# Kernel tuning notes

Hardware: AMD Instinct MI355X
Metric: run time of the kernel (lower is better)

The kernel has to match this reference:

```python
import jax, jax.numpy as jnp
import numpy as np

B, N, D, NS, ITERS = 64, 4096, 256, 8, 3
EPS_ATTN = 1e-5   # module eps (added to attn)
EPS_LN = 1e-5     # torch LayerNorm default eps


def layer_norm(x, g, b):
    m = jnp.mean(x, axis=-1, keepdims=True)
    v = jnp.mean((x - m) ** 2, axis=-1, keepdims=True)
    return (x - m) / jnp.sqrt(v + EPS_LN) * g + b


def setup_inputs() -> dict:
    key = jax.random.key(0)
    ks = jax.random.split(key, 16)
    s = 0.02
    return {
        "inputs": jax.random.normal(ks[0], (B, N, D), jnp.float32),
        "slots_init": jax.random.normal(ks[1], (1, NS, D), jnp.float32),
        "Wq": jax.random.normal(ks[2], (D, D), jnp.float32) * s,
        "Wk": jax.random.normal(ks[3], (D, D), jnp.float32) * s,
        "Wv": jax.random.normal(ks[4], (D, D), jnp.float32) * s,
        "W_ih": jax.random.normal(ks[5], (3 * D, D), jnp.float32) * s,
        "W_hh": jax.random.normal(ks[6], (3 * D, D), jnp.float32) * s,
        "b_ih": jnp.zeros((3 * D,), jnp.float32),
        "b_hh": jnp.zeros((3 * D,), jnp.float32),
        "ln_in_g": jnp.ones((D,), jnp.float32),
        "ln_in_b": jnp.zeros((D,), jnp.float32),
        "ln_s_g": jnp.ones((D,), jnp.float32),
        "ln_s_b": jnp.zeros((D,), jnp.float32),
        "ln_m_g": jnp.ones((D,), jnp.float32),
        "ln_m_b": jnp.zeros((D,), jnp.float32),
        "W1": jax.random.normal(ks[7], (4 * D, D), jnp.float32) * s,
        "b1": jnp.zeros((4 * D,), jnp.float32),
        "W2": jax.random.normal(ks[8], (D, 4 * D), jnp.float32) * s,
        "b2": jnp.zeros((D,), jnp.float32),
    }


def gru_cell(x, h, W_ih, W_hh, b_ih, b_hh):
    # x, h: [M, D]; PyTorch GRU cell equations (gate order r, z, n)
    gi = x @ W_ih.T + b_ih
    gh = h @ W_hh.T + b_hh
    gi_r, gi_z, gi_n = jnp.split(gi, 3, axis=-1)
    gh_r, gh_z, gh_n = jnp.split(gh, 3, axis=-1)
    r = jax.nn.sigmoid(gi_r + gh_r)
    z = jax.nn.sigmoid(gi_z + gh_z)
    n = jnp.tanh(gi_n + r * gh_n)
    return (1.0 - z) * n + z * h


def reference(inputs, slots_init, Wq, Wk, Wv, W_ih, W_hh, b_ih, b_hh,
              ln_in_g, ln_in_b, ln_s_g, ln_s_b, ln_m_g, ln_m_b,
              W1, b1, W2, b2):
    b, n, d = inputs.shape
    scale = d ** -0.5
    slots = jnp.broadcast_to(slots_init, (b, NS, d))

    x = layer_norm(inputs, ln_in_g, ln_in_b)
    k = x @ Wk.T  # [b, n, d]
    v = x @ Wv.T  # [b, n, d]

    for _ in range(ITERS):
        slots_prev = slots
        s_n = layer_norm(slots, ln_s_g, ln_s_b)
        q = s_n @ Wq.T  # [b, ns, d]
        dots = jnp.einsum('bid,bjd->bij', q, k) * scale  # [b, ns, n]
        attn = jax.nn.softmax(dots, axis=1) + EPS_ATTN   # softmax over slots
        attn = attn / jnp.mean(attn, axis=-1, keepdims=True)
        updates = jnp.einsum('bjd,bij->bid', v, attn)     # [b, ns, d]
        h = gru_cell(updates.reshape(-1, d), slots_prev.reshape(-1, d),
                     W_ih, W_hh, b_ih, b_hh)
        slots = h.reshape(b, NS, d)
        # residual MLP with pre-norm
        y = layer_norm(slots, ln_m_g, ln_m_b)
        y = jax.nn.leaky_relu(y @ W1.T + b1, negative_slope=0.01)
        slots = slots + (y @ W2.T + b2)
    return slots
```

## Files before the change

### kernel.cpp

```cpp
#include <hip/hip_runtime.h>
#include <hip/hip_fp16.h>
#include <hip/hip_bf16.h>


#define BB 64
#define NN 4096
#define DD 256
#define NSL 8
#define NITER 3

__device__ __forceinline__ float wredsum(float v){
#pragma unroll
  for(int m=32;m;m>>=1) v += __shfl_xor(v, m, 64);
  return v;
}
__device__ __forceinline__ float2 u2f2(unsigned u){ __half2 h; __builtin_memcpy(&h,&u,4); return __half22float2(h); }
__device__ __forceinline__ float sigm(float v){ return 1.0f/(1.0f+__expf(-v)); }

union U4 { uint4 u; __half2 h[4]; };

__global__ __launch_bounds__(256) void k_prep(
    const float* __restrict__ Whh, const float* __restrict__ W1,
    const float* __restrict__ W2,  const float* __restrict__ sinit,
    __half* __restrict__ Wg, __half* __restrict__ W1t, __half* __restrict__ W2t,
    float* __restrict__ slots){
  for(int idx=blockIdx.x*256+threadIdx.x; idx<851968; idx+=gridDim.x*256){
    if(idx<196608){ int col=idx>>8, c=idx&255; Wg[(size_t)c*1536+768+col]=__float2half(Whh[idx]); }
    else if(idx<458752){ int k=idx-196608; int col=k>>8, c=k&255; W1t[(size_t)c*1024+col]=__float2half(W1[k]); }
    else if(idx<720896){ int k=idx-458752; int col=k>>10, c=k&1023; W2t[(size_t)c*256+col]=__float2half(W2[k]); }
    else { int k=idx-720896; slots[k]=sinit[k&2047]; }
  }
}

__global__ __launch_bounds__(256) void k_WC(const float* __restrict__ Wih, const float* __restrict__ Wv,
                                            __half* __restrict__ Wg){
  int col=blockIdx.x;
  int t=threadIdx.x;
  __shared__ float wr[256];
  wr[t]=Wih[col*256+t];
  __syncthreads();
  float acc=0.f;
#pragma unroll 8
  for(int d=0;d<256;d++) acc += wr[d]*Wv[d*256+t];
  Wg[(size_t)t*1536+col]=__float2half(acc);
}

__global__ __launch_bounds__(256) void k_M(const float* __restrict__ Wq, const float* __restrict__ Wk,
                                           __half* __restrict__ M2h){
  int c = blockIdx.x, e = threadIdx.x;
  float acc = 0.f;
#pragma unroll 8
  for(int d=0; d<256; d++) acc += Wq[d*256+e]*Wk[d*256+c];
  M2h[c*256+e] = __float2half(acc * 0.0625f);
}

__global__ __launch_bounds__(256) void k_ln_x(const float* __restrict__ in, const float* __restrict__ g,
                                              const float* __restrict__ bbv, __half* __restrict__ x){
  int row  = blockIdx.x*4 + (threadIdx.x>>6);
  int lane = threadIdx.x&63;
  const float4 v = ((const float4*)(in + (size_t)row*DD))[lane];
  float s  = v.x+v.y+v.z+v.w;
  float ss = v.x*v.x+v.y*v.y+v.z*v.z+v.w*v.w;
  s = wredsum(s); ss = wredsum(ss);
  float m = s*(1.0f/256.0f);
  float r = rsqrtf(ss*(1.0f/256.0f) - m*m + 1e-5f);
  float4 gv = ((const float4*)g)[lane];
  float4 bv = ((const float4*)bbv)[lane];
  float y0=(v.x-m)*r*gv.x+bv.x, y1=(v.y-m)*r*gv.y+bv.y;
  float y2=(v.z-m)*r*gv.z+bv.z, y3=(v.w-m)*r*gv.w+bv.w;
  __half2 h0=__floats2half2_rn(y0,y1), h1=__floats2half2_rn(y2,y3);
  uint2 u; __builtin_memcpy(&u.x,&h0,4); __builtin_memcpy(&u.y,&h1,4);
  ((uint2*)(x + (size_t)row*DD))[lane] = u;
}

__global__ __launch_bounds__(256) void k_pre(const float* __restrict__ slots, const float* __restrict__ g,
                                             const float* __restrict__ bbv, const __half* __restrict__ M2h,
                                             float* __restrict__ qs){
  int row = blockIdx.x;
  int t = threadIdx.x;
  __shared__ __align__(16) float sn[256];
  __shared__ float red[8];
  float v = slots[row*256 + t];
  float s = wredsum(v), ss = wredsum(v*v);
  int wid=t>>6, lane=t&63;
  if(lane==0){ red[wid]=s; red[4+wid]=ss; }
  __syncthreads();
  float S  = red[0]+red[1]+red[2]+red[3];
  float SS = red[4]+red[5]+red[6]+red[7];
  float m = S*(1.0f/256.0f);
  float r = rsqrtf(SS*(1.0f/256.0f) - m*m + 1e-5f);
  sn[t] = (v-m)*r*g[t]+bbv[t];
  __syncthreads();
  const uint4* w4 = (const uint4*)(M2h + (size_t)t*256);
  float acc=0.f;
#pragma unroll 4
  for(int kk=0;kk<32;kk++){
    U4 w; w.u=w4[kk];
#pragma unroll
    for(int q=0;q<4;q++){
      float2 f=__half22float2(w.h[q]);
      acc += sn[kk*8+2*q]*f.x + sn[kk*8+2*q+1]*f.y;
    }
  }
  qs[row*256+t]=acc;
}

__global__ __launch_bounds__(256) void k_att(const __half* __restrict__ x, const float* __restrict__ qs,
                                             float* __restrict__ pagg){
  int b = blockIdx.x>>4;
  int t = threadIdx.x;
  size_t j = (size_t)blockIdx.x*256 + t;
  __shared__ __align__(16) float qt[256][8];
  __shared__ __align__(16) float wl[256][8];
  __shared__ __align__(16) float aggl[4][2048];
  __shared__ float wsl[4][8];
  const float* qb = qs + b*2048;
  for(int e=t;e<2048;e+=256) qt[e&255][e>>8]=qb[e];
  __syncthreads();
  const uint4* xr = (const uint4*)(x + j*DD);
  float pd[8]={0,0,0,0,0,0,0,0};
#pragma unroll 2
  for(int ch=0; ch<32; ch++){
    uint4 u = xr[ch];
    float2 f0=u2f2(u.x), f1=u2f2(u.y), f2=u2f2(u.z), f3=u2f2(u.w);
    float xv[8]={f0.x,f0.y,f1.x,f1.y,f2.x,f2.y,f3.x,f3.y};
    int c0=ch*8;
#pragma unroll
    for(int cc=0;cc<8;cc++){
      const float4* qp=(const float4*)&qt[c0+cc][0];
      float4 qa=qp[0], qc=qp[1];
      float xvv=xv[cc];
      pd[0]+=qa.x*xvv; pd[1]+=qa.y*xvv; pd[2]+=qa.z*xvv; pd[3]+=qa.w*xvv;
      pd[4]+=qc.x*xvv; pd[5]+=qc.y*xvv; pd[6]+=qc.z*xvv; pd[7]+=qc.w*xvv;
    }
  }
  float mx=pd[0];
#pragma unroll
  for(int i=1;i<8;i++) mx=fmaxf(mx,pd[i]);
  float ev[8]; float ssum=0.f;
#pragma unroll
  for(int i=0;i<8;i++){ ev[i]=__expf(pd[i]-mx); ssum+=ev[i]; }
  float inv=1.0f/ssum;
#pragma unroll
  for(int i=0;i<8;i++) wl[t][i]=ev[i]*inv+1e-5f;
  __syncthreads();
  int wid=t>>6, lane=t&63;
  float acc[8][4];
#pragma unroll
  for(int i=0;i<8;i++){ acc[i][0]=0;acc[i][1]=0;acc[i][2]=0;acc[i][3]=0; }
  float ws[8]={0,0,0,0,0,0,0,0};
  for(int r=0;r<64;r++){
    int jl = wid*64 + r;
    uint2 u = ((const uint2*)(x + ((size_t)blockIdx.x*256 + jl)*DD))[lane];
    float2 f01=u2f2(u.x), f23=u2f2(u.y);
    const float4* wp=(const float4*)&wl[jl][0];
    float4 wa=wp[0], wb_=wp[1];
    float wv[8]={wa.x,wa.y,wa.z,wa.w,wb_.x,wb_.y,wb_.z,wb_.w};
    float xv[4]={f01.x,f01.y,f23.x,f23.y};
#pragma unroll
    for(int i=0;i<8;i++){
      acc[i][0]+=wv[i]*xv[0]; acc[i][1]+=wv[i]*xv[1];
      acc[i][2]+=wv[i]*xv[2]; acc[i][3]+=wv[i]*xv[3];
      ws[i]+=wv[i];
    }
  }
#pragma unroll
  for(int i=0;i<8;i++){
    float4 st={acc[i][0],acc[i][1],acc[i][2],acc[i][3]};
    *((float4*)&aggl[wid][i*256 + lane*4])=st;
  }
  if(lane==0){
#pragma unroll
    for(int i=0;i<8;i++) wsl[wid][i]=ws[i];
  }
  __syncthreads();
  float* pb = pagg + (size_t)blockIdx.x*2064;
  for(int e=t;e<2048;e+=256) pb[e]=aggl[0][e]+aggl[1][e]+aggl[2][e]+aggl[3][e];
  if(t<8) pb[2048+t]=wsl[0][t]+wsl[1][t]+wsl[2][t]+wsl[3][t];
}

__global__ __launch_bounds__(512) void t_gates2(
    const float* __restrict__ pagg, const float* __restrict__ slots_in,
    const __half* __restrict__ Wg, const float* __restrict__ bih, const float* __restrict__ bhh,
    const float* __restrict__ lm_g, const float* __restrict__ lm_b,
    float* __restrict__ hb, __half* __restrict__ ysh){
  int row0=blockIdx.x*2;
  int b=row0>>3, i0=row0&7;
  int t=threadIdx.x;
  int r=t>>8, c=t&255;
  __shared__ float AS[4][256];
  __shared__ __align__(16) float gl[2][1536];
  __shared__ float fac[2];
  __shared__ float redS[2][4], redQ[2][4];
  const float* pb = pagg + (size_t)b*16*2064;
  {
    float s=0.f;
#pragma unroll
    for(int ch=0;ch<16;ch++) s += pb[ch*2064 + (i0+r)*256 + c];
    AS[r][c]=s;
    AS[2+r][c]=slots_in[(size_t)(row0+r)*256+c];
  }
  if(t<2){
    float s=0.f;
#pragma unroll
    for(int ch=0;ch<16;ch++) s += pb[ch*2064 + 2048 + i0 + t];
    fac[t]=4096.0f/s;
  }
  __syncthreads();
  AS[r][c] *= fac[r];
  __syncthreads();
  if(t<384){
    int c0=t*4;
    bool ih = c0<768;
    const float* X0 = ih? AS[0] : AS[2];
    const float* X1 = ih? AS[1] : AS[3];
    const __half* wb = Wg + c0;
    float a00=0,a01=0,a02=0,a03=0, a10=0,a11=0,a12=0,a13=0;
#pragma unroll 8
    for(int k=0;k<256;k++){
      uint2 u = *(const uint2*)(wb + (size_t)k*1536);
      float2 f0=u2f2(u.x), f1=u2f2(u.y);
      float x0=X0[k], x1=X1[k];
      a00+=x0*f0.x; a01+=x0*f0.y; a02+=x0*f1.x; a03+=x0*f1.y;
      a10+=x1*f0.x; a11+=x1*f0.y; a12+=x1*f1.x; a13+=x1*f1.y;
    }
    const float* bb = ih? bih : bhh;
    int bc = ih? c0 : c0-768;
    float4 bv=*(const float4*)&bb[bc];
    gl[0][c0]=a00+bv.x; gl[0][c0+1]=a01+bv.y; gl[0][c0+2]=a02+bv.z; gl[0][c0+3]=a03+bv.w;
    gl[1][c0]=a10+bv.x; gl[1][c0+1]=a11+bv.y; gl[1][c0+2]=a12+bv.z; gl[1][c0+3]=a13+bv.w;
  }
  __syncthreads();
  {
    float gir=gl[r][c], giz=gl[r][256+c], gin=gl[r][512+c];
    float ghr=gl[r][768+c], ghz=gl[r][1024+c], ghn=gl[r][1280+c];
    float hp=AS[2+r][c];
    float rr=sigm(gir+ghr), z=sigm(giz+ghz);
    float n=tanhf(gin+rr*ghn);
    float hv=(1.0f-z)*n+z*hp;
    hb[(size_t)(row0+r)*256+c]=hv;
    float s=wredsum(hv), ss=wredsum(hv*hv);
    if((t&63)==0){ redS[r][(t>>6)&3]=s; redQ[r][(t>>6)&3]=ss; }
    __syncthreads();
    float S_=redS[r][0]+redS[r][1]+redS[r][2]+redS[r][3];
    float SS=redQ[r][0]+redQ[r][1]+redQ[r][2]+redQ[r][3];
    float m=S_*(1.0f/256.0f);
    float rs=rsqrtf(SS*(1.0f/256.0f)-m*m+1e-5f);
    ysh[(size_t)(row0+r)*256+c]=__float2half((hv-m)*rs*lm_g[c]+lm_b[c]);
  }
}

__global__ __launch_bounds__(512) void t_mlp(
    const float* __restrict__ hb, const __half* __restrict__ ysg,
    const __half* __restrict__ W1t, const float* __restrict__ b1,
    const __half* __restrict__ W2t, const float* __restrict__ b2,
    const float* __restrict__ ls_g, const float* __restrict__ ls_b,
    const __half* __restrict__ M2h,
    float* __restrict__ dst, float* __restrict__ qs, int last){
  int row0=blockIdx.x*2;
  int t=threadIdx.x;
  int r=t>>8, c=t&255;
  __shared__ float ys[2][256];
  __shared__ __align__(16) float pz[2][2][1024];
  __shared__ __align__(16) float z1[2][1024];
  __shared__ float pm[2][4][256];
  __shared__ float redS[2][4], redQ[2][4];
  ys[r][c]=__half2float(ysg[(size_t)(row0+r)*256+c]);
  __syncthreads();
  {
    int c0=c*4;
    const __half* wb = W1t + (size_t)r*128*1024 + c0;
    float a00=0,a01=0,a02=0,a03=0, a10=0,a11=0,a12=0,a13=0;
#pragma unroll 8
    for(int k=0;k<128;k++){
      uint2 u=*(const uint2*)(wb + (size_t)k*1024);
      float2 f0=u2f2(u.x), f1=u2f2(u.y);
      float x0=ys[0][r*128+k], x1=ys[1][r*128+k];
      a00+=x0*f0.x; a01+=x0*f0.y; a02+=x0*f1.x; a03+=x0*f1.y;
      a10+=x1*f0.x; a11+=x1*f0.y; a12+=x1*f1.x; a13+=x1*f1.y;
    }
    pz[r][0][c0]=a00; pz[r][0][c0+1]=a01; pz[r][0][c0+2]=a02; pz[r][0][c0+3]=a03;
    pz[r][1][c0]=a10; pz[r][1][c0+1]=a11; pz[r][1][c0+2]=a12; pz[r][1][c0+3]=a13;
  }
  __syncthreads();
  for(int idx=t; idx<2048; idx+=512){
    int rr2=idx>>10, cc=idx&1023;
    float v=pz[0][rr2][cc]+pz[1][rr2][cc]+b1[cc];
    z1[rr2][cc]= v>0.f? v : 0.01f*v;
  }
  __syncthreads();
  if(t<256){
    int ks4=t>>6, cg=t&63;
    int c0=cg*4;
    const __half* wb = W2t + (size_t)ks4*256*256 + c0;
    float a00=0,a01=0,a02=0,a03=0, a10=0,a11=0,a12=0,a13=0;
#pragma unroll 8
    for(int k=0;k<256;k++){
      uint2 u=*(const uint2*)(wb + (size_t)k*256);
      float2 f0=u2f2(u.x), f1=u2f2(u.y);
      float x0=z1[0][ks4*256+k], x1=z1[1][ks4*256+k];
      a00+=x0*f0.x; a01+=x0*f0.y; a02+=x0*f1.x; a03+=x0*f1.y;
      a10+=x1*f0.x; a11+=x1*f0.y; a12+=x1*f1.x; a13+=x1*f1.y;
    }
    pm[0][ks4][c0]=a00; pm[0][ks4][c0+1]=a01; pm[0][ks4][c0+2]=a02; pm[0][ks4][c0+3]=a03;
    pm[1][ks4][c0]=a10; pm[1][ks4][c0+1]=a11; pm[1][ks4][c0+2]=a12; pm[1][ks4][c0+3]=a13;
  }
  __syncthreads();
  float s = hb[(size_t)(row0+r)*256+c] + pm[r][0][c]+pm[r][1][c]+pm[r][2][c]+pm[r][3][c] + b2[c];
  dst[(size_t)(row0+r)*256+c]=s;
  if(last) return;
  float su=wredsum(s), sq=wredsum(s*s);
  if((t&63)==0){ redS[r][(t>>6)&3]=su; redQ[r][(t>>6)&3]=sq; }
  __syncthreads();
  float S_=redS[r][0]+redS[r][1]+redS[r][2]+redS[r][3];
  float SS=redQ[r][0]+redQ[r][1]+redQ[r][2]+redQ[r][3];
  float m=S_*(1.0f/256.0f);
  float rs=rsqrtf(SS*(1.0f/256.0f)-m*m+1e-5f);
  ys[r][c]=(s-m)*rs*ls_g[c]+ls_b[c];
  __syncthreads();
  {
    const uint4* m4=(const uint4*)(M2h+(size_t)c*256);
    float acc=0.f;
#pragma unroll 4
    for(int kk=0;kk<32;kk++){
      U4 w; w.u=m4[kk];
#pragma unroll
      for(int q=0;q<4;q++){
        float2 f=__half22float2(w.h[q]);
        acc += ys[r][kk*8+2*q]*f.x + ys[r][kk*8+2*q+1]*f.y;
      }
    }
    qs[(size_t)(row0+r)*256+c]=acc;
  }
}

extern "C" void kernel_launch(void* const* d_in, const int* in_sizes, int n_in,
                              void* d_out, int out_size, void* d_ws, size_t ws_size,
                              hipStream_t stream){
  const float* inputs=(const float*)d_in[0];
  const float* sinit =(const float*)d_in[1];
  const float* Wq =(const float*)d_in[2];
  const float* Wk =(const float*)d_in[3];
  const float* Wv =(const float*)d_in[4];
  const float* Wih=(const float*)d_in[5];
  const float* Whh=(const float*)d_in[6];
  const float* bih=(const float*)d_in[7];
  const float* bhh=(const float*)d_in[8];
  const float* lin_g=(const float*)d_in[9];
  const float* lin_b=(const float*)d_in[10];
  const float* ls_g=(const float*)d_in[11];
  const float* ls_b=(const float*)d_in[12];
  const float* lm_g=(const float*)d_in[13];
  const float* lm_b=(const float*)d_in[14];
  const float* W1=(const float*)d_in[15];
  const float* b1=(const float*)d_in[16];
  const float* W2=(const float*)d_in[17];
  const float* b2=(const float*)d_in[18];

  char* w=(char*)d_ws;
  __half* x    =(__half*)w; w += (size_t)BB*NN*DD*2;
  float* qs    =(float*)w;  w += 512*256*4;
  float* slots =(float*)w;  w += 512*256*4;
  float* pagg  =(float*)w;  w += (size_t)1024*2064*4;
  __half* M2h  =(__half*)w; w += 256*256*2;
  __half* Wg   =(__half*)w; w += 256*1536*2;
  __half* W1t  =(__half*)w; w += 256*1024*2;
  __half* W2t  =(__half*)w; w += 1024*256*2;
  float* hb    =(float*)w;  w += 512*256*4;
  __half* ysh  =(__half*)w; w += 512*256*2;

  hipLaunchKernelGGL(k_prep, dim3(1664), dim3(256), 0, stream,
                     Whh, W1, W2, sinit, Wg, W1t, W2t, slots);
  hipLaunchKernelGGL(k_WC,   dim3(768),  dim3(256), 0, stream, Wih, Wv, Wg);
  hipLaunchKernelGGL(k_M,    dim3(256),  dim3(256), 0, stream, Wq, Wk, M2h);
  hipLaunchKernelGGL(k_ln_x, dim3(65536),dim3(256), 0, stream, inputs, lin_g, lin_b, x);
  hipLaunchKernelGGL(k_pre,  dim3(512),  dim3(256), 0, stream, slots, ls_g, ls_b, M2h, qs);
  for(int it=0; it<NITER; ++it){
    int last = (it==NITER-1);
    float* dst = last ? (float*)d_out : slots;
    hipLaunchKernelGGL(k_att,    dim3(1024), dim3(256), 0, stream, x, qs, pagg);
    hipLaunchKernelGGL(t_gates2, dim3(256),  dim3(512), 0, stream, pagg, slots, Wg, bih, bhh,
                       lm_g, lm_b, hb, ysh);
    hipLaunchKernelGGL(t_mlp,    dim3(256),  dim3(512), 0, stream, hb, ysh, W1t, b1, W2t, b2,
                       ls_g, ls_b, M2h, dst, qs, last);
  }
}
```

Baseline: 462.2 us.

## Fuse slot-attention iterations into one cooperative persistent kernel with grid syncs

Replaces the per-iteration k_att, t_gates2 and t_mlp launches plus k_pre with a single cooperative kernel. It uses grid.sync between the attention phase and the per-row GRU/MLP phase, and interleaves the weights into k-pair-major half2 layouts for coalesced per-thread column loads. The attention aggregation now loops over rows with a strided x column access per thread, and each block processes one slot row instead of two. This removes launch gaps and intermediate buffers, but grid syncs and fewer rows per block lower reuse of the weight loads.

```diff
diff --git a/kernel.cpp b/kernel.cpp
--- a/kernel.cpp
+++ b/kernel.cpp
@@ -1,6 +1,9 @@
 #include <hip/hip_runtime.h>
 #include <hip/hip_fp16.h>
 #include <hip/hip_bf16.h>
+#include <hip/hip_cooperative_groups.h>
+
+namespace cg = cooperative_groups;
 
 
 #define BB 64
@@ -17,23 +20,29 @@
 __device__ __forceinline__ float2 u2f2(unsigned u){ __half2 h; __builtin_memcpy(&h,&u,4); return __half22float2(h); }
 __device__ __forceinline__ float sigm(float v){ return 1.0f/(1.0f+__expf(-v)); }
 
-union U4 { uint4 u; __half2 h[4]; };
-
 __global__ __launch_bounds__(256) void k_prep(
     const float* __restrict__ Whh, const float* __restrict__ W1,
     const float* __restrict__ W2,  const float* __restrict__ sinit,
-    __half* __restrict__ Wg, __half* __restrict__ W1t, __half* __restrict__ W2t,
+    __half* __restrict__ Wgp, __half* __restrict__ W1p, __half* __restrict__ W2p,
     float* __restrict__ slots){
   for(int idx=blockIdx.x*256+threadIdx.x; idx<851968; idx+=gridDim.x*256){
-    if(idx<196608){ int col=idx>>8, c=idx&255; Wg[(size_t)c*1536+768+col]=__float2half(Whh[idx]); }
-    else if(idx<458752){ int k=idx-196608; int col=k>>8, c=k&255; W1t[(size_t)c*1024+col]=__float2half(W1[k]); }
-    else if(idx<720896){ int k=idx-458752; int col=k>>10, c=k&1023; W2t[(size_t)c*256+col]=__float2half(W2[k]); }
-    else { int k=idx-720896; slots[k]=sinit[k&2047]; }
+    if(idx<196608){
+      int col=idx>>8, k=idx&255; int g=3+(col>>8), c=col&255;
+      Wgp[(((size_t)g*128+(k>>1))*256+c)*2+(k&1)] = __float2half(Whh[idx]);
+    } else if(idx<458752){
+      int k2=idx-196608; int col=k2>>8, k=k2&255; int g=col>>8, c=col&255;
+      W1p[(((size_t)g*128+(k>>1))*256+c)*2+(k&1)] = __float2half(W1[k2]);
+    } else if(idx<720896){
+      int k3=idx-458752; int col=k3>>10, k=k3&1023;
+      W2p[(((size_t)(k>>1))*256+col)*2+(k&1)] = __float2half(W2[k3]);
+    } else {
+      int k4=idx-720896; slots[k4]=sinit[k4&2047];
+    }
   }
 }
 
 __global__ __launch_bounds__(256) void k_WC(const float* __restrict__ Wih, const float* __restrict__ Wv,
-                                            __half* __restrict__ Wg){
+                                            __half* __restrict__ Wgp){
   int col=blockIdx.x;
   int t=threadIdx.x;
   __shared__ float wr[256];
@@ -42,16 +51,17 @@
   float acc=0.f;
 #pragma unroll 8
   for(int d=0;d<256;d++) acc += wr[d]*Wv[d*256+t];
-  Wg[(size_t)t*1536+col]=__float2half(acc);
+  int g=col>>8, c=col&255;
+  Wgp[(((size_t)g*128+(t>>1))*256+c)*2+(t&1)] = __float2half(acc);
 }
 
 __global__ __launch_bounds__(256) void k_M(const float* __restrict__ Wq, const float* __restrict__ Wk,
-                                           __half* __restrict__ M2h){
+                                           __half* __restrict__ Mp){
   int c = blockIdx.x, e = threadIdx.x;
   float acc = 0.f;
 #pragma unroll 8
   for(int d=0; d<256; d++) acc += Wq[d*256+e]*Wk[d*256+c];
-  M2h[c*256+e] = __float2half(acc * 0.0625f);
+  Mp[(((size_t)(e>>1))*256+c)*2+(e&1)] = __float2half(acc * 0.0625f);
 }
 
 __global__ __launch_bounds__(256) void k_ln_x(const float* __restrict__ in, const float* __restrict__ g,
@@ -73,264 +83,201 @@
   ((uint2*)(x + (size_t)row*DD))[lane] = u;
 }
 
-__global__ __launch_bounds__(256) void k_pre(const float* __restrict__ slots, const float* __restrict__ g,
-                                             const float* __restrict__ bbv, const __half* __restrict__ M2h,
-                                             float* __restrict__ qs){
-  int row = blockIdx.x;
-  int t = threadIdx.x;
-  __shared__ __align__(16) float sn[256];
-  __shared__ float red[8];
-  float v = slots[row*256 + t];
-  float s = wredsum(v), ss = wredsum(v*v);
-  int wid=t>>6, lane=t&63;
-  if(lane==0){ red[wid]=s; red[4+wid]=ss; }
-  __syncthreads();
-  float S  = red[0]+red[1]+red[2]+red[3];
-  float SS = red[4]+red[5]+red[6]+red[7];
-  float m = S*(1.0f/256.0f);
-  float r = rsqrtf(SS*(1.0f/256.0f) - m*m + 1e-5f);
-  sn[t] = (v-m)*r*g[t]+bbv[t];
-  __syncthreads();
-  const uint4* w4 = (const uint4*)(M2h + (size_t)t*256);
-  float acc=0.f;
-#pragma unroll 4
-  for(int kk=0;kk<32;kk++){
-    U4 w; w.u=w4[kk];
-#pragma unroll
-    for(int q=0;q<4;q++){
-      float2 f=__half22float2(w.h[q]);
-      acc += sn[kk*8+2*q]*f.x + sn[kk*8+2*q+1]*f.y;
-    }
-  }
-  qs[row*256+t]=acc;
-}
-
-__global__ __launch_bounds__(256) void k_att(const __half* __restrict__ x, const float* __restrict__ qs,
-                                             float* __restrict__ pagg){
-  int b = blockIdx.x>>4;
-  int t = threadIdx.x;
-  size_t j = (size_t)blockIdx.x*256 + t;
+__global__ __launch_bounds__(256, 4) void k_main(
+    const __half* __restrict__ x, float* __restrict__ qs, float* __restrict__ slots,
+    float* __restrict__ pagg,
+    const __half* __restrict__ Wgp, const __half* __restrict__ W1p,
+    const __half* __restrict__ W2p, const __half* __restrict__ Mp,
+    const float* __restrict__ bih, const float* __restrict__ bhh,
+    const float* __restrict__ lm_g, const float* __restrict__ lm_b,
+    const float* __restrict__ b1, const float* __restrict__ b2,
+    const float* __restrict__ ls_g, const float* __restrict__ ls_b,
+    float* __restrict__ out){
+  cg::grid_group grid = cg::this_grid();
+  const int blk=blockIdx.x, t=threadIdx.x, G=gridDim.x;
+  const int wid=t>>6, lane=t&63;
   __shared__ __align__(16) float qt[256][8];
   __shared__ __align__(16) float wl[256][8];
-  __shared__ __align__(16) float aggl[4][2048];
   __shared__ float wsl[4][8];
-  const float* qb = qs + b*2048;
-  for(int e=t;e<2048;e+=256) qt[e&255][e>>8]=qb[e];
-  __syncthreads();
-  const uint4* xr = (const uint4*)(x + j*DD);
-  float pd[8]={0,0,0,0,0,0,0,0};
+  __shared__ float aggS[256], slS[256], ysl[256];
+  __shared__ __align__(16) float z1l[1024];
+  __shared__ float redS[4], redQ[4], facS, f16S[16];
+  const __half2* Wg2=(const __half2*)Wgp;
+  const __half2* W12=(const __half2*)W1p;
+  const __half2* W22=(const __half2*)W2p;
+  const __half2* Mp2=(const __half2*)Mp;
+
+  for(int row=blk; row<512; row+=G){
+    __syncthreads();
+    float v = slots[(size_t)row*256+t];
+    float s=wredsum(v), ss=wredsum(v*v);
+    if(lane==0){ redS[wid]=s; redQ[wid]=ss; }
+    __syncthreads();
+    float S=redS[0]+redS[1]+redS[2]+redS[3];
+    float SS=redQ[0]+redQ[1]+redQ[2]+redQ[3];
+    float m=S*(1.0f/256.0f);
+    float rs=rsqrtf(SS*(1.0f/256.0f)-m*m+1e-5f);
+    ysl[t]=(v-m)*rs*ls_g[t]+ls_b[t];
+    __syncthreads();
+    float acc=0.f;
+#pragma unroll 8
+    for(int k2=0;k2<128;k2++){
+      float2 f=__half22float2(Mp2[(size_t)k2*256+t]);
+      acc += f.x*ysl[2*k2] + f.y*ysl[2*k2+1];
+    }
+    qs[(size_t)row*256+t]=acc;
+  }
+  grid.sync();
+
+  for(int it=0; it<NITER; ++it){
+    const int last = (it==NITER-1);
+    for(int ab=blk; ab<1024; ab+=G){
+      __syncthreads();
+      int b = ab>>4;
+      const float* qb = qs + (size_t)b*2048;
+      for(int e=t;e<2048;e+=256) qt[e&255][e>>8]=qb[e];
+      __syncthreads();
+      size_t j = (size_t)ab*256 + t;
+      const uint4* xr = (const uint4*)(x + j*DD);
+      float pd[8]={0,0,0,0,0,0,0,0};
 #pragma unroll 2
-  for(int ch=0; ch<32; ch++){
-    uint4 u = xr[ch];
-    float2 f0=u2f2(u.x), f1=u2f2(u.y), f2=u2f2(u.z), f3=u2f2(u.w);
-    float xv[8]={f0.x,f0.y,f1.x,f1.y,f2.x,f2.y,f3.x,f3.y};
-    int c0=ch*8;
-#pragma unroll
-    for(int cc=0;cc<8;cc++){
-      const float4* qp=(const float4*)&qt[c0+cc][0];
-      float4 qa=qp[0], qc=qp[1];
-      float xvv=xv[cc];
-      pd[0]+=qa.x*xvv; pd[1]+=qa.y*xvv; pd[2]+=qa.z*xvv; pd[3]+=qa.w*xvv;
-      pd[4]+=qc.x*xvv; pd[5]+=qc.y*xvv; pd[6]+=qc.z*xvv; pd[7]+=qc.w*xvv;
+      for(int ch=0; ch<32; ch++){
+        uint4 u = xr[ch];
+        float2 f0=u2f2(u.x), f1=u2f2(u.y), f2=u2f2(u.z), f3=u2f2(u.w);
+        float xv[8]={f0.x,f0.y,f1.x,f1.y,f2.x,f2.y,f3.x,f3.y};
+        int c0=ch*8;
+#pragma unroll
+        for(int cc=0;cc<8;cc++){
+          const float4* qp=(const float4*)&qt[c0+cc][0];
+          float4 qa=qp[0], qc=qp[1];
+          float xvv=xv[cc];
+          pd[0]+=qa.x*xvv; pd[1]+=qa.y*xvv; pd[2]+=qa.z*xvv; pd[3]+=qa.w*xvv;
+          pd[4]+=qc.x*xvv; pd[5]+=qc.y*xvv; pd[6]+=qc.z*xvv; pd[7]+=qc.w*xvv;
+        }
+      }
+      float mx=pd[0];
+#pragma unroll
+      for(int i=1;i<8;i++) mx=fmaxf(mx,pd[i]);
+      float w[8]; float ssum=0.f;
+#pragma unroll
+      for(int i=0;i<8;i++){ w[i]=__expf(pd[i]-mx); ssum+=w[i]; }
+      float inv=1.0f/ssum;
+#pragma unroll
+      for(int i=0;i<8;i++){ w[i]=w[i]*inv+1e-5f; wl[t][i]=w[i]; }
+#pragma unroll
+      for(int i=0;i<8;i++){
+        float s=wredsum(w[i]);
+        if(lane==0) wsl[wid][i]=s;
+      }
+      __syncthreads();
+      if(t<8) pagg[(size_t)ab*2064 + 2048 + t] = wsl[0][t]+wsl[1][t]+wsl[2][t]+wsl[3][t];
+      int c = wid*64 + lane;
+      float acc[8]={0,0,0,0,0,0,0,0};
+      const __half* xb = x + (size_t)ab*256*DD + c;
+#pragma unroll 4
+      for(int j2=0;j2<256;j2++){
+        float xv = __half2float(xb[(size_t)j2*DD]);
+        const float4* wp=(const float4*)&wl[j2][0];
+        float4 w0=wp[0], w1=wp[1];
+        acc[0]+=w0.x*xv; acc[1]+=w0.y*xv; acc[2]+=w0.z*xv; acc[3]+=w0.w*xv;
+        acc[4]+=w1.x*xv; acc[5]+=w1.y*xv; acc[6]+=w1.z*xv; acc[7]+=w1.w*xv;
+      }
+#pragma unroll
+      for(int i=0;i<8;i++) pagg[(size_t)ab*2064 + i*256 + c] = acc[i];
     }
-  }
-  float mx=pd[0];
-#pragma unroll
-  for(int i=1;i<8;i++) mx=fmaxf(mx,pd[i]);
-  float ev[8]; float ssum=0.f;
-#pragma unroll
-  for(int i=0;i<8;i++){ ev[i]=__expf(pd[i]-mx); ssum+=ev[i]; }
-  float inv=1.0f/ssum;
-#pragma unroll
-  for(int i=0;i<8;i++) wl[t][i]=ev[i]*inv+1e-5f;
-  __syncthreads();
-  int wid=t>>6, lane=t&63;
-  float acc[8][4];
-#pragma unroll
-  for(int i=0;i<8;i++){ acc[i][0]=0;acc[i][1]=0;acc[i][2]=0;acc[i][3]=0; }
-  float ws[8]={0,0,0,0,0,0,0,0};
-  for(int r=0;r<64;r++){
-    int jl = wid*64 + r;
-    uint2 u = ((const uint2*)(x + ((size_t)blockIdx.x*256 + jl)*DD))[lane];
-    float2 f01=u2f2(u.x), f23=u2f2(u.y);
-    const float4* wp=(const float4*)&wl[jl][0];
-    float4 wa=wp[0], wb_=wp[1];
-    float wv[8]={wa.x,wa.y,wa.z,wa.w,wb_.x,wb_.y,wb_.z,wb_.w};
-    float xv[4]={f01.x,f01.y,f23.x,f23.y};
-#pragma unroll
-    for(int i=0;i<8;i++){
-      acc[i][0]+=wv[i]*xv[0]; acc[i][1]+=wv[i]*xv[1];
-      acc[i][2]+=wv[i]*xv[2]; acc[i][3]+=wv[i]*xv[3];
-      ws[i]+=wv[i];
+    grid.sync();
+    float* dst = last ? out : slots;
+    for(int row=blk; row<512; row+=G){
+      __syncthreads();
+      int b=row>>3, i0=row&7;
+      const float* pb = pagg + (size_t)b*16*2064;
+      float s=0.f;
+#pragma unroll
+      for(int ch=0;ch<16;ch++) s += pb[ch*2064 + i0*256 + t];
+      if(t<16) f16S[t]=pb[t*2064 + 2048 + i0];
+      float hp = slots[(size_t)row*256+t];
+      slS[t]=hp;
+      __syncthreads();
+      float wsum=0.f;
+#pragma unroll
+      for(int k2=0;k2<16;k2++) wsum+=f16S[k2];
+      aggS[t]=s*(4096.0f/wsum);
+      __syncthreads();
+      float a0=0,a1=0,a2=0,a3=0,a4=0,a5=0;
+#pragma unroll 8
+      for(int k2=0;k2<128;k2++){
+        float xa0=aggS[2*k2], xa1=aggS[2*k2+1];
+        float xs0=slS[2*k2],  xs1=slS[2*k2+1];
+        float2 f0=__half22float2(Wg2[(size_t)(0*128+k2)*256+t]);
+        float2 f1=__half22float2(Wg2[(size_t)(1*128+k2)*256+t]);
+        float2 f2=__half22float2(Wg2[(size_t)(2*128+k2)*256+t]);
+        float2 f3=__half22float2(Wg2[(size_t)(3*128+k2)*256+t]);
+        float2 f4=__half22float2(Wg2[(size_t)(4*128+k2)*256+t]);
+        float2 f5=__half22float2(Wg2[(size_t)(5*128+k2)*256+t]);
+        a0+=f0.x*xa0+f0.y*xa1; a1+=f1.x*xa0+f1.y*xa1; a2+=f2.x*xa0+f2.y*xa1;
+        a3+=f3.x*xs0+f3.y*xs1; a4+=f4.x*xs0+f4.y*xs1; a5+=f5.x*xs0+f5.y*xs1;
+      }
+      float gir=a0+bih[t], giz=a1+bih[256+t], gin=a2+bih[512+t];
+      float ghr=a3+bhh[t], ghz=a4+bhh[256+t], ghn=a5+bhh[512+t];
+      float rr=sigm(gir+ghr), z=sigm(giz+ghz);
+      float n=tanhf(gin+rr*ghn);
+      float hv=(1.0f-z)*n + z*hp;
+      float s1=wredsum(hv), q1=wredsum(hv*hv);
+      if(lane==0){ redS[wid]=s1; redQ[wid]=q1; }
+      __syncthreads();
+      float S=redS[0]+redS[1]+redS[2]+redS[3];
+      float SS=redQ[0]+redQ[1]+redQ[2]+redQ[3];
+      float m=S*(1.0f/256.0f);
+      float rs=rsqrtf(SS*(1.0f/256.0f)-m*m+1e-5f);
+      ysl[t]=(hv-m)*rs*lm_g[t]+lm_b[t];
+      __syncthreads();
+      float m0=0,m1=0,m2=0,m3=0;
+#pragma unroll 8
+      for(int k2=0;k2<128;k2++){
+        float y0=ysl[2*k2], y1=ysl[2*k2+1];
+        float2 f0=__half22float2(W12[(size_t)(0*128+k2)*256+t]);
+        float2 f1=__half22float2(W12[(size_t)(1*128+k2)*256+t]);
+        float2 f2=__half22float2(W12[(size_t)(2*128+k2)*256+t]);
+        float2 f3=__half22float2(W12[(size_t)(3*128+k2)*256+t]);
+        m0+=f0.x*y0+f0.y*y1; m1+=f1.x*y0+f1.y*y1;
+        m2+=f2.x*y0+f2.y*y1; m3+=f3.x*y0+f3.y*y1;
+      }
+      {
+        float v0=m0+b1[t];      z1l[t]      = v0>0.f?v0:0.01f*v0;
+        float v1=m1+b1[256+t];  z1l[256+t]  = v1>0.f?v1:0.01f*v1;
+        float v2=m2+b1[512+t];  z1l[512+t]  = v2>0.f?v2:0.01f*v2;
+        float v3=m3+b1[768+t];  z1l[768+t]  = v3>0.f?v3:0.01f*v3;
+      }
+      __syncthreads();
+      float o=0.f;
+#pragma unroll 8
+      for(int k2=0;k2<512;k2++){
+        float2 f=__half22float2(W22[(size_t)k2*256+t]);
+        o += f.x*z1l[2*k2] + f.y*z1l[2*k2+1];
+      }
+      float sv = hv + o + b2[t];
+      dst[(size_t)row*256+t]=sv;
+      if(!last){
+        float s2=wredsum(sv), q2=wredsum(sv*sv);
+        __syncthreads();
+        if(lane==0){ redS[wid]=s2; redQ[wid]=q2; }
+        __syncthreads();
+        float S2=redS[0]+redS[1]+redS[2]+redS[3];
+        float SS2=redQ[0]+redQ[1]+redQ[2]+redQ[3];
+        float m2_=S2*(1.0f/256.0f);
+        float rs2=rsqrtf(SS2*(1.0f/256.0f)-m2_*m2_+1e-5f);
+        ysl[t]=(sv-m2_)*rs2*ls_g[t]+ls_b[t];
+        __syncthreads();
+        float acc=0.f;
+#pragma unroll 8
+        for(int k2=0;k2<128;k2++){
+          float2 f=__half22float2(Mp2[(size_t)k2*256+t]);
+          acc += f.x*ysl[2*k2] + f.y*ysl[2*k2+1];
+        }
+        qs[(size_t)row*256+t]=acc;
+      }
     }
-  }
-#pragma unroll
-  for(int i=0;i<8;i++){
-    float4 st={acc[i][0],acc[i][1],acc[i][2],acc[i][3]};
-    *((float4*)&aggl[wid][i*256 + lane*4])=st;
-  }
-  if(lane==0){
-#pragma unroll
-    for(int i=0;i<8;i++) wsl[wid][i]=ws[i];
-  }
-  __syncthreads();
-  float* pb = pagg + (size_t)blockIdx.x*2064;
-  for(int e=t;e<2048;e+=256) pb[e]=aggl[0][e]+aggl[1][e]+aggl[2][e]+aggl[3][e];
-  if(t<8) pb[2048+t]=wsl[0][t]+wsl[1][t]+wsl[2][t]+wsl[3][t];
-}
-
-__global__ __launch_bounds__(512) void t_gates2(
-    const float* __restrict__ pagg, const float* __restrict__ slots_in,
-    const __half* __restrict__ Wg, const float* __restrict__ bih, const float* __restrict__ bhh,
-    const float* __restrict__ lm_g, const float* __restrict__ lm_b,
-    float* __restrict__ hb, __half* __restrict__ ysh){
-  int row0=blockIdx.x*2;
-  int b=row0>>3, i0=row0&7;
-  int t=threadIdx.x;
-  int r=t>>8, c=t&255;
-  __shared__ float AS[4][256];
-  __shared__ __align__(16) float gl[2][1536];
-  __shared__ float fac[2];
-  __shared__ float redS[2][4], redQ[2][4];
-  const float* pb = pagg + (size_t)b*16*2064;
-  {
-    float s=0.f;
-#pragma unroll
-    for(int ch=0;ch<16;ch++) s += pb[ch*2064 + (i0+r)*256 + c];
-    AS[r][c]=s;
-    AS[2+r][c]=slots_in[(size_t)(row0+r)*256+c];
-  }
-  if(t<2){
-    float s=0.f;
-#pragma unroll
-    for(int ch=0;ch<16;ch++) s += pb[ch*2064 + 2048 + i0 + t];
-    fac[t]=4096.0f/s;
-  }
-  __syncthreads();
-  AS[r][c] *= fac[r];
-  __syncthreads();
-  if(t<384){
-    int c0=t*4;
-    bool ih = c0<768;
-    const float* X0 = ih? AS[0] : AS[2];
-    const float* X1 = ih? AS[1] : AS[3];
-    const __half* wb = Wg + c0;
-    float a00=0,a01=0,a02=0,a03=0, a10=0,a11=0,a12=0,a13=0;
-#pragma unroll 8
-    for(int k=0;k<256;k++){
-      uint2 u = *(const uint2*)(wb + (size_t)k*1536);
-      float2 f0=u2f2(u.x), f1=u2f2(u.y);
-      float x0=X0[k], x1=X1[k];
-      a00+=x0*f0.x; a01+=x0*f0.y; a02+=x0*f1.x; a03+=x0*f1.y;
-      a10+=x1*f0.x; a11+=x1*f0.y; a12+=x1*f1.x; a13+=x1*f1.y;
-    }
-    const float* bb = ih? bih : bhh;
-    int bc = ih? c0 : c0-768;
-    float4 bv=*(const float4*)&bb[bc];
-    gl[0][c0]=a00+bv.x; gl[0][c0+1]=a01+bv.y; gl[0][c0+2]=a02+bv.z; gl[0][c0+3]=a03+bv.w;
-    gl[1][c0]=a10+bv.x; gl[1][c0+1]=a11+bv.y; gl[1][c0+2]=a12+bv.z; gl[1][c0+3]=a13+bv.w;
-  }
-  __syncthreads();
-  {
-    float gir=gl[r][c], giz=gl[r][256+c], gin=gl[r][512+c];
-    float ghr=gl[r][768+c], ghz=gl[r][1024+c], ghn=gl[r][1280+c];
-    float hp=AS[2+r][c];
-    float rr=sigm(gir+ghr), z=sigm(giz+ghz);
-    float n=tanhf(gin+rr*ghn);
-    float hv=(1.0f-z)*n+z*hp;
-    hb[(size_t)(row0+r)*256+c]=hv;
-    float s=wredsum(hv), ss=wredsum(hv*hv);
-    if((t&63)==0){ redS[r][(t>>6)&3]=s; redQ[r][(t>>6)&3]=ss; }
-    __syncthreads();
-    float S_=redS[r][0]+redS[r][1]+redS[r][2]+redS[r][3];
-    float SS=redQ[r][0]+redQ[r][1]+redQ[r][2]+redQ[r][3];
-    float m=S_*(1.0f/256.0f);
-    float rs=rsqrtf(SS*(1.0f/256.0f)-m*m+1e-5f);
-    ysh[(size_t)(row0+r)*256+c]=__float2half((hv-m)*rs*lm_g[c]+lm_b[c]);
-  }
-}
-
-__global__ __launch_bounds__(512) void t_mlp(
-    const float* __restrict__ hb, const __half* __restrict__ ysg,
-    const __half* __restrict__ W1t, const float* __restrict__ b1,
-    const __half* __restrict__ W2t, const float* __restrict__ b2,
-    const float* __restrict__ ls_g, const float* __restrict__ ls_b,
-    const __half* __restrict__ M2h,
-    float* __restrict__ dst, float* __restrict__ qs, int last){
-  int row0=blockIdx.x*2;
-  int t=threadIdx.x;
-  int r=t>>8, c=t&255;
-  __shared__ float ys[2][256];
-  __shared__ __align__(16) float pz[2][2][1024];
-  __shared__ __align__(16) float z1[2][1024];
-  __shared__ float pm[2][4][256];
-  __shared__ float redS[2][4], redQ[2][4];
-  ys[r][c]=__half2float(ysg[(size_t)(row0+r)*256+c]);
-  __syncthreads();
-  {
-    int c0=c*4;
-    const __half* wb = W1t + (size_t)r*128*1024 + c0;
-    float a00=0,a01=0,a02=0,a03=0, a10=0,a11=0,a12=0,a13=0;
-#pragma unroll 8
-    for(int k=0;k<128;k++){
-      uint2 u=*(const uint2*)(wb + (size_t)k*1024);
-      float2 f0=u2f2(u.x), f1=u2f2(u.y);
-      float x0=ys[0][r*128+k], x1=ys[1][r*128+k];
-      a00+=x0*f0.x; a01+=x0*f0.y; a02+=x0*f1.x; a03+=x0*f1.y;
-      a10+=x1*f0.x; a11+=x1*f0.y; a12+=x1*f1.x; a13+=x1*f1.y;
-    }
-    pz[r][0][c0]=a00; pz[r][0][c0+1]=a01; pz[r][0][c0+2]=a02; pz[r][0][c0+3]=a03;
-    pz[r][1][c0]=a10; pz[r][1][c0+1]=a11; pz[r][1][c0+2]=a12; pz[r][1][c0+3]=a13;
-  }
-  __syncthreads();
-  for(int idx=t; idx<2048; idx+=512){
-    int rr2=idx>>10, cc=idx&1023;
-    float v=pz[0][rr2][cc]+pz[1][rr2][cc]+b1[cc];
-    z1[rr2][cc]= v>0.f? v : 0.01f*v;
-  }
-  __syncthreads();
-  if(t<256){
-    int ks4=t>>6, cg=t&63;
-    int c0=cg*4;
-    const __half* wb = W2t + (size_t)ks4*256*256 + c0;
-    float a00=0,a01=0,a02=0,a03=0, a10=0,a11=0,a12=0,a13=0;
-#pragma unroll 8
-    for(int k=0;k<256;k++){
-      uint2 u=*(const uint2*)(wb + (size_t)k*256);
-      float2 f0=u2f2(u.x), f1=u2f2(u.y);
-      float x0=z1[0][ks4*256+k], x1=z1[1][ks4*256+k];
-      a00+=x0*f0.x; a01+=x0*f0.y; a02+=x0*f1.x; a03+=x0*f1.y;
-      a10+=x1*f0.x; a11+=x1*f0.y; a12+=x1*f1.x; a13+=x1*f1.y;
-    }
-    pm[0][ks4][c0]=a00; pm[0][ks4][c0+1]=a01; pm[0][ks4][c0+2]=a02; pm[0][ks4][c0+3]=a03;
-    pm[1][ks4][c0]=a10; pm[1][ks4][c0+1]=a11; pm[1][ks4][c0+2]=a12; pm[1][ks4][c0+3]=a13;
-  }
-  __syncthreads();
-  float s = hb[(size_t)(row0+r)*256+c] + pm[r][0][c]+pm[r][1][c]+pm[r][2][c]+pm[r][3][c] + b2[c];
-  dst[(size_t)(row0+r)*256+c]=s;
-  if(last) return;
-  float su=wredsum(s), sq=wredsum(s*s);
-  if((t&63)==0){ redS[r][(t>>6)&3]=su; redQ[r][(t>>6)&3]=sq; }
-  __syncthreads();
-  float S_=redS[r][0]+redS[r][1]+redS[r][2]+redS[r][3];
-  float SS=redQ[r][0]+redQ[r][1]+redQ[r][2]+redQ[r][3];
-  float m=S_*(1.0f/256.0f);
-  float rs=rsqrtf(SS*(1.0f/256.0f)-m*m+1e-5f);
-  ys[r][c]=(s-m)*rs*ls_g[c]+ls_b[c];
-  __syncthreads();
-  {
-    const uint4* m4=(const uint4*)(M2h+(size_t)c*256);
-    float acc=0.f;
-#pragma unroll 4
-    for(int kk=0;kk<32;kk++){
-      U4 w; w.u=m4[kk];
-#pragma unroll
-      for(int q=0;q<4;q++){
-        float2 f=__half22float2(w.h[q]);
-        acc += ys[r][kk*8+2*q]*f.x + ys[r][kk*8+2*q+1]*f.y;
-      }
-    }
-    qs[(size_t)(row0+r)*256+c]=acc;
+    if(!last) grid.sync();
   }
 }
 
@@ -362,26 +309,31 @@
   float* qs    =(float*)w;  w += 512*256*4;
   float* slots =(float*)w;  w += 512*256*4;
   float* pagg  =(float*)w;  w += (size_t)1024*2064*4;
-  __half* M2h  =(__half*)w; w += 256*256*2;
-  __half* Wg   =(__half*)w; w += 256*1536*2;
-  __half* W1t  =(__half*)w; w += 256*1024*2;
-  __half* W2t  =(__half*)w; w += 1024*256*2;
-  float* hb    =(float*)w;  w += 512*256*4;
-  __half* ysh  =(__half*)w; w += 512*256*2;
+  __half* Wgp  =(__half*)w; w += (size_t)6*128*256*2*2;
+  __half* W1p  =(__half*)w; w += (size_t)4*128*256*2*2;
+  __half* W2p  =(__half*)w; w += (size_t)512*256*2*2;
+  __half* Mp   =(__half*)w; w += (size_t)128*256*2*2;
 
   hipLaunchKernelGGL(k_prep, dim3(1664), dim3(256), 0, stream,
-                     Whh, W1, W2, sinit, Wg, W1t, W2t, slots);
-  hipLaunchKernelGGL(k_WC,   dim3(768),  dim3(256), 0, stream, Wih, Wv, Wg);
-  hipLaunchKernelGGL(k_M,    dim3(256),  dim3(256), 0, stream, Wq, Wk, M2h);
+                     Whh, W1, W2, sinit, Wgp, W1p, W2p, slots);
+  hipLaunchKernelGGL(k_WC,   dim3(768),  dim3(256), 0, stream, Wih, Wv, Wgp);
+  hipLaunchKernelGGL(k_M,    dim3(256),  dim3(256), 0, stream, Wq, Wk, Mp);
   hipLaunchKernelGGL(k_ln_x, dim3(65536),dim3(256), 0, stream, inputs, lin_g, lin_b, x);
-  hipLaunchKernelGGL(k_pre,  dim3(512),  dim3(256), 0, stream, slots, ls_g, ls_b, M2h, qs);
-  for(int it=0; it<NITER; ++it){
-    int last = (it==NITER-1);
-    float* dst = last ? (float*)d_out : slots;
-    hipLaunchKernelGGL(k_att,    dim3(1024), dim3(256), 0, stream, x, qs, pagg);
-    hipLaunchKernelGGL(t_gates2, dim3(256),  dim3(512), 0, stream, pagg, slots, Wg, bih, bhh,
-                       lm_g, lm_b, hb, ysh);
-    hipLaunchKernelGGL(t_mlp,    dim3(256),  dim3(512), 0, stream, hb, ysh, W1t, b1, W2t, b2,
-                       ls_g, ls_b, M2h, dst, qs, last);
-  }
-}
+
+  int nb=0;
+  hipError_t e = hipOccupancyMaxActiveBlocksPerMultiprocessor(&nb, k_main, 256, 0);
+  if(e!=hipSuccess || nb<1) nb=1;
+  if(nb>4) nb=4;
+  int gridN = nb*256; if(gridN>1024) gridN=1024;
+
+  const __half* xc=x; const __half* Wgc=Wgp; const __half* W1c=W1p;
+  const __half* W2c=W2p; const __half* Mpc=Mp;
+  float* outp=(float*)d_out;
+  void* args[] = {
+    (void*)&xc, (void*)&qs, (void*)&slots, (void*)&pagg,
+    (void*)&Wgc, (void*)&W1c, (void*)&W2c, (void*)&Mpc,
+    (void*)&bih, (void*)&bhh, (void*)&lm_g, (void*)&lm_b,
+    (void*)&b1, (void*)&b2, (void*)&ls_g, (void*)&ls_b, (void*)&outp
+  };
+  hipLaunchCooperativeKernel((void*)k_main, dim3(gridN), dim3(256), args, 0, stream);
+}
```

Result: slower. 1.107 ms (+139.5%).
